# Performance work log

Measured on AMD Instinct MI355X. Metric: run time of the kernel, lower is better.

The kernel has to match this reference:

```python
import jax, jax.numpy as jnp
import numpy as np

B, S, DM, H, D = 2, 2048, 1024, 16, 64

def setup_inputs() -> dict:
    key = jax.random.key(0)
    ks = jax.random.split(key, 9)
    def g(k, shape, scale=0.02):
        return jax.random.normal(k, shape, dtype=jnp.float32) * scale
    return {
        "x":  jax.random.normal(ks[0], (B, S, DM), dtype=jnp.float32),
        "Wq": g(ks[1], (DM, H * D)), "bq": g(ks[2], (H * D,)),
        "Wk": g(ks[3], (DM, H * D)), "bk": g(ks[4], (H * D,)),
        "Wv": g(ks[5], (DM, H * D)), "bv": g(ks[6], (H * D,)),
        "Wo": g(ks[7], (H * D, DM)), "bo": g(ks[8], (DM,)),
    }

def reference(x, Wq, bq, Wk, bk, Wv, bv, Wo, bo):
    b, s, _ = x.shape
    # projections -> (B, H, S, D)
    q = (x @ Wq + bq).reshape(b, s, H, D).transpose(0, 2, 1, 3)
    k = (x @ Wk + bk).reshape(b, s, H, D).transpose(0, 2, 1, 3)
    v = (x @ Wv + bv).reshape(b, s, H, D).transpose(0, 2, 1, 3)
    # naive attention: full (B,H,S,S) scores, causal mask, softmax
    scores = jnp.einsum("bhqd,bhkd->bhqk", q, k) / jnp.sqrt(jnp.float32(D))
    causal = jnp.tril(jnp.ones((s, s), dtype=bool))
    scores = jnp.where(causal[None, None], scores, jnp.float32(-jnp.inf))
    weights = jax.nn.softmax(scores, axis=-1)
    out = jnp.einsum("bhqk,bhkd->bhqd", weights, v)  # (B,H,S,D)
    out = out.transpose(0, 2, 1, 3).reshape(b, s, H * D)
    return out @ Wo + bo  # dropout_p = 0 -> identity
```

## Files before the change

### kernel.cpp

```cpp
#include <hip/hip_runtime.h>
#include <hip/hip_bf16.h>

typedef __hip_bfloat16 bf16;
typedef __attribute__((ext_vector_type(8))) short bf16x8;
typedef __attribute__((ext_vector_type(4))) float f32x4;
typedef __attribute__((ext_vector_type(4))) unsigned int u32x4;

#define MFMA_BF16(a, b, c) __builtin_amdgcn_mfma_f32_16x16x32_bf16((a), (b), (c), 0, 0, 0)

static constexpr int B_  = 2;
static constexpr int S_  = 2048;
static constexpr int DM_ = 1024;
static constexpr int H_  = 16;
static constexpr int D_  = 64;
static constexpr int M_  = B_ * S_;

__device__ __forceinline__ void load16(const void* g, void* l) {
  __builtin_amdgcn_global_load_lds(
      (const __attribute__((address_space(1))) void*)g,
      (__attribute__((address_space(3))) void*)l, 16, 0, 0);
}

__device__ __forceinline__ unsigned int pack_bf16(float lo, float hi) {
  const unsigned int ul = __builtin_bit_cast(unsigned short, __float2bfloat16(lo));
  const unsigned int uh = __builtin_bit_cast(unsigned short, __float2bfloat16(hi));
  return (uh << 16) | ul;
}


__global__ void cvt_f32_bf16_kernel(const float* __restrict__ in,
                                    bf16* __restrict__ out, int n4) {
  int i = blockIdx.x * blockDim.x + threadIdx.x;
  if (i >= n4) return;
  float4 v = ((const float4*)in)[i];
  ushort4 u;
  u.x = __builtin_bit_cast(unsigned short, __float2bfloat16(v.x));
  u.y = __builtin_bit_cast(unsigned short, __float2bfloat16(v.y));
  u.z = __builtin_bit_cast(unsigned short, __float2bfloat16(v.z));
  u.w = __builtin_bit_cast(unsigned short, __float2bfloat16(v.w));
  ((ushort4*)out)[i] = u;
}

__global__ void transpose_cvt_kernel(const float* __restrict__ w0,
                                     const float* __restrict__ w1,
                                     const float* __restrict__ w2,
                                     const float* __restrict__ w3,
                                     bf16* __restrict__ o0, bf16* __restrict__ o1,
                                     bf16* __restrict__ o2, bf16* __restrict__ o3) {
  __shared__ float t[32][33];
  const float* in = blockIdx.z == 0 ? w0 : blockIdx.z == 1 ? w1 : blockIdx.z == 2 ? w2 : w3;
  bf16* out = blockIdx.z == 0 ? o0 : blockIdx.z == 1 ? o1 : blockIdx.z == 2 ? o2 : o3;
  int tx = threadIdx.x & 31;
  int ty = threadIdx.x >> 5;
  int r0 = blockIdx.y * 32;
  int c0 = blockIdx.x * 32;
#pragma unroll
  for (int yy = 0; yy < 32; yy += 8)
    t[ty + yy][tx] = in[(size_t)(r0 + ty + yy) * DM_ + c0 + tx];
  __syncthreads();
#pragma unroll
  for (int yy = 0; yy < 32; yy += 8)
    out[(size_t)(c0 + ty + yy) * DM_ + r0 + tx] = __float2bfloat16(t[tx][ty + yy]);
}

template <int MODE>
__global__ __launch_bounds__(256) void gemm_bt_kernel(
    const bf16* __restrict__ A, const bf16* __restrict__ Bt,
    const float* __restrict__ bias, const float* __restrict__ bias2,
    const float* __restrict__ bias3, void* __restrict__ out, int K) {
  __shared__ bf16 As[2][128 * 32];
  __shared__ bf16 Bs[2][128 * 32];
  const int tid = threadIdx.x;
  const int wid = tid >> 6, lane = tid & 63;
  const int g = lane >> 4, c = lane & 15;
  const int wr = wid >> 1, wc = wid & 1;
  const int bm = blockIdx.x, bn = blockIdx.y;

  f32x4 acc[4][4] = {};

  const char* Ag = (const char*)(A + (size_t)bm * 128 * K);
  const char* Bg = (const char*)(Bt + (size_t)bn * 128 * K);
  const int f0 = tid * 16, f1 = f0 + 4096;
  const int r0 = f0 >> 6, cb0 = f0 & 63;
  const int r1 = f1 >> 6;
  const size_t rowbytes = (size_t)K * 2;

  auto stage = [&](int kt, int bufi) {
    const size_t koff = (size_t)kt * 64;
    load16(Ag + (size_t)r0 * rowbytes + koff + cb0, (char*)As[bufi] + f0);
    load16(Ag + (size_t)r1 * rowbytes + koff + cb0, (char*)As[bufi] + f1);
    load16(Bg + (size_t)r0 * rowbytes + koff + cb0, (char*)Bs[bufi] + f0);
    load16(Bg + (size_t)r1 * rowbytes + koff + cb0, (char*)Bs[bufi] + f1);
  };

  const int NT = K / 32;
  stage(0, 0);
  int cur = 0;
#pragma unroll 1
  for (int kt = 0; kt < NT; ++kt) {
    if (kt + 1 < NT) {
      stage(kt + 1, cur ^ 1);
      asm volatile("s_waitcnt vmcnt(4)" ::: "memory");
    } else {
      asm volatile("s_waitcnt vmcnt(0)" ::: "memory");
    }
    __builtin_amdgcn_s_barrier();

    bf16x8 af[4], bfr[4];
#pragma unroll
    for (int mi = 0; mi < 4; ++mi)
      af[mi] = *(const bf16x8*)&As[cur][(wr * 64 + mi * 16 + c) * 32 + g * 8];
#pragma unroll
    for (int ni = 0; ni < 4; ++ni)
      bfr[ni] = *(const bf16x8*)&Bs[cur][(wc * 64 + ni * 16 + c) * 32 + g * 8];
    __builtin_amdgcn_s_setprio(1);
#pragma unroll
    for (int mi = 0; mi < 4; ++mi)
#pragma unroll
      for (int ni = 0; ni < 4; ++ni)
        acc[mi][ni] = MFMA_BF16(af[mi], bfr[ni], acc[mi][ni]);
    __builtin_amdgcn_s_setprio(0);

    if (kt + 1 < NT) __builtin_amdgcn_s_barrier();
    cur ^= 1;
  }

#pragma unroll
  for (int ni = 0; ni < 4; ++ni) {
    const int n_g = bn * 128 + wc * 64 + ni * 16 + c;
    float bv;
    if constexpr (MODE == 3) {
      const int proj = n_g >> 10, ncol = n_g & 1023;
      bv = proj == 0 ? bias[ncol] : proj == 1 ? bias2[ncol] : bias3[ncol];
    } else {
      bv = bias[n_g];
    }
#pragma unroll
    for (int mi = 0; mi < 4; ++mi) {
#pragma unroll
      for (int r = 0; r < 4; ++r) {
        const int m_g = bm * 128 + wr * 64 + mi * 16 + g * 4 + r;
        const float val = acc[mi][ni][r] + bv;
        if constexpr (MODE == 2) {
          ((float*)out)[(size_t)m_g * DM_ + n_g] = val;
        } else {
          const int proj = n_g >> 10, ncol = n_g & 1023;
          const int b = m_g >> 11, s = m_g & (S_ - 1);
          const int h = ncol >> 6, d = ncol & (D_ - 1);
          size_t idx = (size_t)proj * 4194304;
          if (proj < 2)
            idx += (((size_t)(b * H_ + h)) * S_ + s) * D_ + d;
          else
            idx += (((size_t)(b * H_ + h)) * D_ + d) * S_ + s;
          ((bf16*)out)[idx] = __float2bfloat16(val);
        }
      }
    }
  }
}

__global__ __launch_bounds__(256, 4) void flash_attn_kernel(
    const bf16* __restrict__ Q, const bf16* __restrict__ Kg,
    const bf16* __restrict__ Vt, bf16* __restrict__ Aout) {
  __shared__ bf16 Ks[2][64 * 64];
  __shared__ bf16 Vs[2][64 * 64];
  const int tid = threadIdx.x;
  const int w = tid >> 6, lane = tid & 63;
  const int g = lane >> 4, c = lane & 15;

  const int bid = blockIdx.x;
  const int xcd = bid & 7, loc = bid >> 3;
  const int bh = xcd * 4 + (loc & 3);
  const int j = 31 - (loc >> 2);
  const int t = j * 4 + w;
  const int b = bh >> 4, h = bh & (H_ - 1);

  const float ALPHA2 = 0.125f * 1.44269504f;
  const float THR2 = 11.5f;
  const float NEG_INF = -__builtin_inff();

  const char* Kbase = (const char*)(Kg + (size_t)bh * S_ * D_);
  const char* Vbase = (const char*)(Vt + (size_t)bh * D_ * S_);
  const int s0 = tid, s1 = tid + 256;
  const int sr0 = s0 >> 3, sq0 = ((s0 & 7) ^ (sr0 & 7)) << 4;
  const int sr1 = s1 >> 3, sq1 = ((s1 & 7) ^ (sr1 & 7)) << 4;

  const bf16* Qp = Q + ((size_t)bh * S_ + t * 16 + c) * D_;
  bf16x8 qf[2];
  qf[0] = *(const bf16x8*)&Qp[g * 8];
  qf[1] = *(const bf16x8*)&Qp[32 + g * 8];

  f32x4 o[4] = {};
  float m = -1000.0f;
  float lsum = 0.0f;

  const int rowlim = w * 16 + c;
  const int src0 = ((g & 1) * 2) * 16 + c;
  const int src1 = src0 + 16;
  const bool ghi = (g >= 2);
  const int cs = c & 7;
  int roff[2][4];
#pragma unroll
  for (int kk = 0; kk < 2; ++kk)
#pragma unroll
    for (int n = 0; n < 4; ++n)
      roff[kk][n] = n * 2048 + c * 128 + (((kk * 4 + g) ^ cs) << 4);

  {
    load16(Kbase + sr0 * 128 + sq0, (char*)Ks[0] + s0 * 16);
    load16(Kbase + sr1 * 128 + sq1, (char*)Ks[0] + s1 * 16);
    load16(Vbase + sr0 * 4096 + sq0, (char*)Vs[0] + s0 * 16);
    load16(Vbase + sr1 * 4096 + sq1, (char*)Vs[0] + s1 * 16);
  }
  __syncthreads();

  int cur = 0;
#pragma unroll 1
  for (int kv = 0; kv <= j; ++kv) {
    if (kv < j) {
      const char* Krow = Kbase + (size_t)(kv + 1) * 8192;
      const char* Vcol = Vbase + (size_t)(kv + 1) * 128;
      const int nb = cur ^ 1;
      load16(Krow + sr0 * 128 + sq0, (char*)Ks[nb] + s0 * 16);
      load16(Krow + sr1 * 128 + sq1, (char*)Ks[nb] + s1 * 16);
      load16(Vcol + sr0 * 4096 + sq0, (char*)Vs[nb] + s0 * 16);
      load16(Vcol + sr1 * 4096 + sq1, (char*)Vs[nb] + s1 * 16);
    }

    const char* Kt = (const char*)Ks[cur];
    const char* Vtile = (const char*)Vs[cur];
    bf16x8 kf[2][4];
#pragma unroll
    for (int kk = 0; kk < 2; ++kk)
#pragma unroll
      for (int n = 0; n < 4; ++n)
        kf[kk][n] = *(const bf16x8*)(Kt + roff[kk][n]);

    f32x4 st[4] = {};
    __builtin_amdgcn_s_setprio(1);
#pragma unroll
    for (int n = 0; n < 4; ++n) {
      st[n] = MFMA_BF16(kf[0][n], qf[0], st[n]);
      st[n] = MFMA_BF16(kf[1][n], qf[1], st[n]);
    }
    __builtin_amdgcn_s_setprio(0);

    bf16x8 vf[2][4];
#pragma unroll
    for (int kk = 0; kk < 2; ++kk)
#pragma unroll
      for (int n = 0; n < 4; ++n)
        vf[kk][n] = *(const bf16x8*)(Vtile + roff[kk][n]);

    float a[4][4];
#pragma unroll
    for (int n = 0; n < 4; ++n)
#pragma unroll
      for (int r = 0; r < 4; ++r)
        a[n][r] = fmaf(st[n][r], ALPHA2, -m);
    if (kv == j) {
#pragma unroll
      for (int n = 0; n < 4; ++n)
#pragma unroll
        for (int r = 0; r < 4; ++r)
          if (n * 16 + g * 4 + r > rowlim) a[n][r] = NEG_INF;
    }

    float dm;
    {
      float t0 = fmaxf(fmaxf(a[0][0], a[0][1]), fmaxf(a[0][2], a[0][3]));
      float t1 = fmaxf(fmaxf(a[1][0], a[1][1]), fmaxf(a[1][2], a[1][3]));
      float t2 = fmaxf(fmaxf(a[2][0], a[2][1]), fmaxf(a[2][2], a[2][3]));
      float t3 = fmaxf(fmaxf(a[3][0], a[3][1]), fmaxf(a[3][2], a[3][3]));
      dm = fmaxf(fmaxf(t0, t1), fmaxf(t2, t3));
    }
    dm = fmaxf(dm, __shfl_xor(dm, 16, 64));
    dm = fmaxf(dm, __shfl_xor(dm, 32, 64));

    if (__any(dm > THR2)) {
      const float sh = fmaxf(dm, 0.0f);
      const float sc = __builtin_amdgcn_exp2f(-sh);
      m += sh;
      lsum *= sc;
#pragma unroll
      for (int n = 0; n < 4; ++n)
#pragma unroll
        for (int r = 0; r < 4; ++r) o[n][r] *= sc;
#pragma unroll
      for (int n = 0; n < 4; ++n)
#pragma unroll
        for (int r = 0; r < 4; ++r) a[n][r] -= sh;
    }

    float p[4][4];
#pragma unroll
    for (int n = 0; n < 4; ++n)
#pragma unroll
      for (int r = 0; r < 4; ++r) p[n][r] = __builtin_amdgcn_exp2f(a[n][r]);
    {
      float q0 = (p[0][0] + p[0][1]) + (p[0][2] + p[0][3]);
      float q1 = (p[1][0] + p[1][1]) + (p[1][2] + p[1][3]);
      float q2 = (p[2][0] + p[2][1]) + (p[2][2] + p[2][3]);
      float q3 = (p[3][0] + p[3][1]) + (p[3][2] + p[3][3]);
      lsum += (q0 + q1) + (q2 + q3);
    }

    unsigned int dw[4][2];
#pragma unroll
    for (int n = 0; n < 4; ++n) {
      dw[n][0] = pack_bf16(p[n][0], p[n][1]);
      dw[n][1] = pack_bf16(p[n][2], p[n][3]);
    }

#pragma unroll
    for (int kk = 0; kk < 2; ++kk) {
      unsigned int bb[4];
      {
        unsigned int lo = __shfl(dw[kk * 2][0], src0, 64);
        unsigned int hi = __shfl(dw[kk * 2 + 1][0], src0, 64);
        bb[0] = ghi ? hi : lo;
      }
      {
        unsigned int lo = __shfl(dw[kk * 2][1], src0, 64);
        unsigned int hi = __shfl(dw[kk * 2 + 1][1], src0, 64);
        bb[1] = ghi ? hi : lo;
      }
      {
        unsigned int lo = __shfl(dw[kk * 2][0], src1, 64);
        unsigned int hi = __shfl(dw[kk * 2 + 1][0], src1, 64);
        bb[2] = ghi ? hi : lo;
      }
      {
        unsigned int lo = __shfl(dw[kk * 2][1], src1, 64);
        unsigned int hi = __shfl(dw[kk * 2 + 1][1], src1, 64);
        bb[3] = ghi ? hi : lo;
      }
      u32x4 bbv = {bb[0], bb[1], bb[2], bb[3]};
      bf16x8 pb = __builtin_bit_cast(bf16x8, bbv);
      __builtin_amdgcn_s_setprio(1);
#pragma unroll
      for (int n = 0; n < 4; ++n) o[n] = MFMA_BF16(vf[kk][n], pb, o[n]);
      __builtin_amdgcn_s_setprio(0);
    }

    __syncthreads();
    cur ^= 1;
  }

  lsum += __shfl_xor(lsum, 16, 64);
  lsum += __shfl_xor(lsum, 32, 64);
  const float inv = 1.0f / lsum;

  bf16* Arow = Aout + ((size_t)b * S_ + t * 16 + c) * (H_ * D_) + h * D_;
#pragma unroll
  for (int n = 0; n < 4; ++n) {
    ushort4 u;
    u.x = __builtin_bit_cast(unsigned short, __float2bfloat16(o[n][0] * inv));
    u.y = __builtin_bit_cast(unsigned short, __float2bfloat16(o[n][1] * inv));
    u.z = __builtin_bit_cast(unsigned short, __float2bfloat16(o[n][2] * inv));
    u.w = __builtin_bit_cast(unsigned short, __float2bfloat16(o[n][3] * inv));
    *(ushort4*)&Arow[n * 16 + g * 4] = u;
  }
}


extern "C" void kernel_launch(void* const* d_in, const int* in_sizes, int n_in,
                              void* d_out, int out_size, void* d_ws, size_t ws_size,
                              hipStream_t stream) {
  (void)in_sizes; (void)n_in; (void)out_size; (void)ws_size;
  const float* x  = (const float*)d_in[0];
  const float* Wq = (const float*)d_in[1];
  const float* bq = (const float*)d_in[2];
  const float* Wk = (const float*)d_in[3];
  const float* bk = (const float*)d_in[4];
  const float* Wv = (const float*)d_in[5];
  const float* bv = (const float*)d_in[6];
  const float* Wo = (const float*)d_in[7];
  const float* bo = (const float*)d_in[8];
  float* out = (float*)d_out;

  char* ws = (char*)d_ws;
  bf16* xb  = (bf16*)(ws);
  bf16* Wqt = (bf16*)(ws + (8u << 20));
  bf16* Wkt = (bf16*)(ws + (10u << 20));
  bf16* Wvt = (bf16*)(ws + (12u << 20));
  bf16* Wot = (bf16*)(ws + (14u << 20));
  bf16* Qb  = (bf16*)(ws + (16u << 20));
  bf16* Kb  = (bf16*)(ws + (24u << 20));
  bf16* Vtb = (bf16*)(ws + (32u << 20));
  bf16* Ab  = xb;

  cvt_f32_bf16_kernel<<<4096, 256, 0, stream>>>(x, xb, (M_ * DM_) / 4);
  transpose_cvt_kernel<<<dim3(32, 32, 4), 256, 0, stream>>>(
      Wq, Wk, Wv, Wo, Wqt, Wkt, Wvt, Wot);

  gemm_bt_kernel<3><<<dim3(32, 24), 256, 0, stream>>>(
      xb, Wqt, bq, bk, bv, (void*)Qb, DM_);

  flash_attn_kernel<<<dim3(1024), 256, 0, stream>>>(Qb, Kb, Vtb, Ab);

  gemm_bt_kernel<2><<<dim3(32, 8), 256, 0, stream>>>(
      Ab, Wot, bo, nullptr, nullptr, (void*)out, DM_);
}
```

Before: 121.6 us.

## Split flash attention blocks into 2-wave halves and drop KV double buffering

The attention kernel now launches 2048 blocks of 128 threads, each covering half of a 64-row query tile, in place of 1024 blocks of 256 threads. LDS use per block is halved by removing the double-buffered K/V tiles: each iteration loads the tile synchronously and then waits on a barrier. The aim is finer-grained scheduling and better load balance across the causal triangle, plus higher occupancy. The cost is that each K/V tile is loaded twice as often overall, and load latency is no longer hidden behind compute by prefetching.

```diff
diff --git a/kernel.cpp b/kernel.cpp
--- a/kernel.cpp
+++ b/kernel.cpp
@@ -159,11 +159,11 @@
   }
 }
 
-__global__ __launch_bounds__(256, 4) void flash_attn_kernel(
+__global__ __launch_bounds__(128, 5) void flash_attn_kernel(
     const bf16* __restrict__ Q, const bf16* __restrict__ Kg,
     const bf16* __restrict__ Vt, bf16* __restrict__ Aout) {
-  __shared__ bf16 Ks[2][64 * 64];
-  __shared__ bf16 Vs[2][64 * 64];
+  __shared__ bf16 Ks[64 * 64];
+  __shared__ bf16 Vs[64 * 64];
   const int tid = threadIdx.x;
   const int w = tid >> 6, lane = tid & 63;
   const int g = lane >> 4, c = lane & 15;
@@ -171,8 +171,10 @@
   const int bid = blockIdx.x;
   const int xcd = bid & 7, loc = bid >> 3;
   const int bh = xcd * 4 + (loc & 3);
-  const int j = 31 - (loc >> 2);
-  const int t = j * 4 + w;
+  const int hq = 63 - (loc >> 2);
+  const int j = hq >> 1;
+  const int half = hq & 1;
+  const int t = j * 4 + half * 2 + w;
   const int b = bh >> 4, h = bh & (H_ - 1);
 
   const float ALPHA2 = 0.125f * 1.44269504f;
@@ -181,9 +183,13 @@
 
   const char* Kbase = (const char*)(Kg + (size_t)bh * S_ * D_);
   const char* Vbase = (const char*)(Vt + (size_t)bh * D_ * S_);
-  const int s0 = tid, s1 = tid + 256;
-  const int sr0 = s0 >> 3, sq0 = ((s0 & 7) ^ (sr0 & 7)) << 4;
-  const int sr1 = s1 >> 3, sq1 = ((s1 & 7) ^ (sr1 & 7)) << 4;
+  int srk[4], sqk[4];
+#pragma unroll
+  for (int k = 0; k < 4; ++k) {
+    const int s = tid + k * 128;
+    srk[k] = s >> 3;
+    sqk[k] = ((s & 7) ^ (srk[k] & 7)) << 4;
+  }
 
   const bf16* Qp = Q + ((size_t)bh * S_ + t * 16 + c) * D_;
   bf16x8 qf[2];
@@ -194,7 +200,7 @@
   float m = -1000.0f;
   float lsum = 0.0f;
 
-  const int rowlim = w * 16 + c;
+  const int rowlim = (half * 2 + w) * 16 + c;
   const int src0 = ((g & 1) * 2) * 16 + c;
   const int src1 = src0 + 16;
   const bool ghi = (g >= 2);
@@ -206,35 +212,25 @@
     for (int n = 0; n < 4; ++n)
       roff[kk][n] = n * 2048 + c * 128 + (((kk * 4 + g) ^ cs) << 4);
 
-  {
-    load16(Kbase + sr0 * 128 + sq0, (char*)Ks[0] + s0 * 16);
-    load16(Kbase + sr1 * 128 + sq1, (char*)Ks[0] + s1 * 16);
-    load16(Vbase + sr0 * 4096 + sq0, (char*)Vs[0] + s0 * 16);
-    load16(Vbase + sr1 * 4096 + sq1, (char*)Vs[0] + s1 * 16);
-  }
-  __syncthreads();
-
-  int cur = 0;
 #pragma unroll 1
   for (int kv = 0; kv <= j; ++kv) {
-    if (kv < j) {
-      const char* Krow = Kbase + (size_t)(kv + 1) * 8192;
-      const char* Vcol = Vbase + (size_t)(kv + 1) * 128;
-      const int nb = cur ^ 1;
-      load16(Krow + sr0 * 128 + sq0, (char*)Ks[nb] + s0 * 16);
-      load16(Krow + sr1 * 128 + sq1, (char*)Ks[nb] + s1 * 16);
-      load16(Vcol + sr0 * 4096 + sq0, (char*)Vs[nb] + s0 * 16);
-      load16(Vcol + sr1 * 4096 + sq1, (char*)Vs[nb] + s1 * 16);
-    }
-
-    const char* Kt = (const char*)Ks[cur];
-    const char* Vtile = (const char*)Vs[cur];
+    {
+      const char* Krow = Kbase + (size_t)kv * 8192;
+      const char* Vcol = Vbase + (size_t)kv * 128;
+#pragma unroll
+      for (int k = 0; k < 4; ++k) {
+        load16(Krow + srk[k] * 128 + sqk[k], (char*)Ks + (tid + k * 128) * 16);
+        load16(Vcol + srk[k] * 4096 + sqk[k], (char*)Vs + (tid + k * 128) * 16);
+      }
+    }
+    __syncthreads();
+
     bf16x8 kf[2][4];
 #pragma unroll
     for (int kk = 0; kk < 2; ++kk)
 #pragma unroll
       for (int n = 0; n < 4; ++n)
-        kf[kk][n] = *(const bf16x8*)(Kt + roff[kk][n]);
+        kf[kk][n] = *(const bf16x8*)((const char*)Ks + roff[kk][n]);
 
     f32x4 st[4] = {};
     __builtin_amdgcn_s_setprio(1);
@@ -250,28 +246,28 @@
     for (int kk = 0; kk < 2; ++kk)
 #pragma unroll
       for (int n = 0; n < 4; ++n)
-        vf[kk][n] = *(const bf16x8*)(Vtile + roff[kk][n]);
-
-    float a[4][4];
+        vf[kk][n] = *(const bf16x8*)((const char*)Vs + roff[kk][n]);
+
+    float aa[4][4];
 #pragma unroll
     for (int n = 0; n < 4; ++n)
 #pragma unroll
       for (int r = 0; r < 4; ++r)
-        a[n][r] = fmaf(st[n][r], ALPHA2, -m);
+        aa[n][r] = fmaf(st[n][r], ALPHA2, -m);
     if (kv == j) {
 #pragma unroll
       for (int n = 0; n < 4; ++n)
 #pragma unroll
         for (int r = 0; r < 4; ++r)
-          if (n * 16 + g * 4 + r > rowlim) a[n][r] = NEG_INF;
+          if (n * 16 + g * 4 + r > rowlim) aa[n][r] = NEG_INF;
     }
 
     float dm;
     {
-      float t0 = fmaxf(fmaxf(a[0][0], a[0][1]), fmaxf(a[0][2], a[0][3]));
-      float t1 = fmaxf(fmaxf(a[1][0], a[1][1]), fmaxf(a[1][2], a[1][3]));
-      float t2 = fmaxf(fmaxf(a[2][0], a[2][1]), fmaxf(a[2][2], a[2][3]));
-      float t3 = fmaxf(fmaxf(a[3][0], a[3][1]), fmaxf(a[3][2], a[3][3]));
+      float t0 = fmaxf(fmaxf(aa[0][0], aa[0][1]), fmaxf(aa[0][2], aa[0][3]));
+      float t1 = fmaxf(fmaxf(aa[1][0], aa[1][1]), fmaxf(aa[1][2], aa[1][3]));
+      float t2 = fmaxf(fmaxf(aa[2][0], aa[2][1]), fmaxf(aa[2][2], aa[2][3]));
+      float t3 = fmaxf(fmaxf(aa[3][0], aa[3][1]), fmaxf(aa[3][2], aa[3][3]));
       dm = fmaxf(fmaxf(t0, t1), fmaxf(t2, t3));
     }
     dm = fmaxf(dm, __shfl_xor(dm, 16, 64));
@@ -289,14 +285,14 @@
 #pragma unroll
       for (int n = 0; n < 4; ++n)
 #pragma unroll
-        for (int r = 0; r < 4; ++r) a[n][r] -= sh;
+        for (int r = 0; r < 4; ++r) aa[n][r] -= sh;
     }
 
     float p[4][4];
 #pragma unroll
     for (int n = 0; n < 4; ++n)
 #pragma unroll
-      for (int r = 0; r < 4; ++r) p[n][r] = __builtin_amdgcn_exp2f(a[n][r]);
+      for (int r = 0; r < 4; ++r) p[n][r] = __builtin_amdgcn_exp2f(aa[n][r]);
     {
       float q0 = (p[0][0] + p[0][1]) + (p[0][2] + p[0][3]);
       float q1 = (p[1][0] + p[1][1]) + (p[1][2] + p[1][3]);
@@ -344,7 +340,6 @@
     }
 
     __syncthreads();
-    cur ^= 1;
   }
 
   lsum += __shfl_xor(lsum, 16, 64);
@@ -397,7 +392,7 @@
   gemm_bt_kernel<3><<<dim3(32, 24), 256, 0, stream>>>(
       xb, Wqt, bq, bk, bv, (void*)Qb, DM_);
 
-  flash_attn_kernel<<<dim3(1024), 256, 0, stream>>>(Qb, Kb, Vtb, Ab);
+  flash_attn_kernel<<<dim3(2048), 128, 0, stream>>>(Qb, Kb, Vtb, Ab);
 
   gemm_bt_kernel<2><<<dim3(32, 8), 256, 0, stream>>>(
       Ab, Wot, bo, nullptr, nullptr, (void*)out, DM_);
```

Result: slower. 137.3 us (+12.9%).

## Add 256x256-tile QKV GEMM kernel with swizzled LDS and XCD-aware block remap

Applied to the files above, without the earlier changes.

Replaces the 128x128 QKV projection GEMM with a dedicated 512-thread kernel using 256x256 output tiles, 64-wide K steps, XOR-swizzled LDS layout and loads of the next stage interleaved across four sub-phases. Blocks are remapped so consecutive tiles land on the same XCD for better L2 reuse. The larger tile cuts global reloads of A and B and the swizzle avoids LDS bank conflicts. In exchange it uses 128 KB of LDS per block and many accumulator registers, which limits occupancy and gives only 192 blocks. The output GEMM template is simplified and a flash-attention variable is renamed.

```diff
diff --git a/kernel.cpp b/kernel.cpp
--- a/kernel.cpp
+++ b/kernel.cpp
@@ -63,11 +63,119 @@
     out[(size_t)(c0 + ty + yy) * DM_ + r0 + tx] = __float2bfloat16(t[tx][ty + yy]);
 }
 
-template <int MODE>
+__global__ __launch_bounds__(512, 2) void gemm256_qkv_kernel(
+    const bf16* __restrict__ A, const bf16* __restrict__ Bt,
+    const float* __restrict__ bias, const float* __restrict__ bias2,
+    const float* __restrict__ bias3, bf16* __restrict__ out) {
+  __shared__ bf16 As[2][256 * 64];
+  __shared__ bf16 Bs[2][256 * 64];
+  const int tid = threadIdx.x;
+  const int wid = tid >> 6, lane = tid & 63;
+  const int g = lane >> 4, c = lane & 15;
+  const int wr = wid >> 2, wc = wid & 3;
+
+  const int orig = blockIdx.x;
+  const int wgid = (orig & 7) * 24 + (orig >> 3);
+  const int bm = wgid & 15, bn = wgid >> 4;
+
+  const char* Ag = (const char*)(A + (size_t)bm * 256 * 1024);
+  const char* Bg = (const char*)(Bt + (size_t)bn * 256 * 1024);
+
+  f32x4 acc[8][4] = {};
+
+  auto stage2 = [&](int kt, int bufi, int pp) {
+#pragma unroll
+    for (int l = 0; l < 2; ++l) {
+      const int k = pp * 2 + l;
+      const int s = tid + (k & 3) * 512;
+      const int sr = s >> 3;
+      const int sq = ((s & 7) ^ (sr & 7)) << 4;
+      if (k < 4)
+        load16(Ag + (size_t)sr * 2048 + kt * 128 + sq, (char*)As[bufi] + s * 16);
+      else
+        load16(Bg + (size_t)sr * 2048 + kt * 128 + sq, (char*)Bs[bufi] + s * 16);
+    }
+  };
+
+#pragma unroll
+  for (int pp = 0; pp < 4; ++pp) stage2(0, 0, pp);
+
+  const int c7 = c & 7;
+  int cur = 0;
+#pragma unroll 1
+  for (int kt = 0; kt < 16; ++kt) {
+    if (kt < 15) {
+      stage2(kt + 1, cur ^ 1, 0);
+      asm volatile("s_waitcnt vmcnt(2)" ::: "memory");
+    } else {
+      asm volatile("s_waitcnt vmcnt(0)" ::: "memory");
+    }
+    __builtin_amdgcn_s_barrier();
+
+#pragma unroll
+    for (int p = 0; p < 4; ++p) {
+      const int qr = p >> 1, qc = p & 1;
+      bf16x8 af[4][2], bfr[2][2];
+#pragma unroll
+      for (int mi = 0; mi < 4; ++mi) {
+        const int rb = (wr * 128 + qr * 64 + mi * 16 + c) * 128;
+#pragma unroll
+        for (int kk = 0; kk < 2; ++kk)
+          af[mi][kk] = *(const bf16x8*)((const char*)As[cur] + rb +
+                                        (((kk * 4 + g) ^ c7) << 4));
+      }
+#pragma unroll
+      for (int ni = 0; ni < 2; ++ni) {
+        const int rb = (wc * 64 + qc * 32 + ni * 16 + c) * 128;
+#pragma unroll
+        for (int kk = 0; kk < 2; ++kk)
+          bfr[ni][kk] = *(const bf16x8*)((const char*)Bs[cur] + rb +
+                                         (((kk * 4 + g) ^ c7) << 4));
+      }
+      if (p < 3 && kt < 15) stage2(kt + 1, cur ^ 1, p + 1);
+      __builtin_amdgcn_s_barrier();
+      __builtin_amdgcn_s_setprio(1);
+#pragma unroll
+      for (int mi = 0; mi < 4; ++mi)
+#pragma unroll
+        for (int ni = 0; ni < 2; ++ni)
+#pragma unroll
+          for (int kk = 0; kk < 2; ++kk)
+            acc[qr * 4 + mi][qc * 2 + ni] =
+                MFMA_BF16(af[mi][kk], bfr[ni][kk], acc[qr * 4 + mi][qc * 2 + ni]);
+      __builtin_amdgcn_s_setprio(0);
+      __builtin_amdgcn_s_barrier();
+    }
+    cur ^= 1;
+  }
+
+#pragma unroll
+  for (int ni = 0; ni < 4; ++ni) {
+    const int n_g = bn * 256 + wc * 64 + ni * 16 + c;
+    const int proj = n_g >> 10, ncol = n_g & 1023;
+    const float bv = proj == 0 ? bias[ncol] : proj == 1 ? bias2[ncol] : bias3[ncol];
+    const int h = ncol >> 6, d = ncol & (D_ - 1);
+#pragma unroll
+    for (int mi = 0; mi < 8; ++mi) {
+#pragma unroll
+      for (int rr = 0; rr < 4; ++rr) {
+        const int m_g = bm * 256 + wr * 128 + mi * 16 + g * 4 + rr;
+        const float val = acc[mi][ni][rr] + bv;
+        const int b = m_g >> 11, s = m_g & (S_ - 1);
+        size_t idx = (size_t)proj * 4194304;
+        if (proj < 2)
+          idx += (((size_t)(b * H_ + h)) * S_ + s) * D_ + d;
+        else
+          idx += (((size_t)(b * H_ + h)) * D_ + d) * S_ + s;
+        out[idx] = __float2bfloat16(val);
+      }
+    }
+  }
+}
+
 __global__ __launch_bounds__(256) void gemm_bt_kernel(
     const bf16* __restrict__ A, const bf16* __restrict__ Bt,
-    const float* __restrict__ bias, const float* __restrict__ bias2,
-    const float* __restrict__ bias3, void* __restrict__ out, int K) {
+    const float* __restrict__ bias, float* __restrict__ out, int K) {
   __shared__ bf16 As[2][128 * 32];
   __shared__ bf16 Bs[2][128 * 32];
   const int tid = threadIdx.x;
@@ -128,32 +236,13 @@
 #pragma unroll
   for (int ni = 0; ni < 4; ++ni) {
     const int n_g = bn * 128 + wc * 64 + ni * 16 + c;
-    float bv;
-    if constexpr (MODE == 3) {
-      const int proj = n_g >> 10, ncol = n_g & 1023;
-      bv = proj == 0 ? bias[ncol] : proj == 1 ? bias2[ncol] : bias3[ncol];
-    } else {
-      bv = bias[n_g];
-    }
+    const float bv = bias[n_g];
 #pragma unroll
     for (int mi = 0; mi < 4; ++mi) {
 #pragma unroll
       for (int r = 0; r < 4; ++r) {
         const int m_g = bm * 128 + wr * 64 + mi * 16 + g * 4 + r;
-        const float val = acc[mi][ni][r] + bv;
-        if constexpr (MODE == 2) {
-          ((float*)out)[(size_t)m_g * DM_ + n_g] = val;
-        } else {
-          const int proj = n_g >> 10, ncol = n_g & 1023;
-          const int b = m_g >> 11, s = m_g & (S_ - 1);
-          const int h = ncol >> 6, d = ncol & (D_ - 1);
-          size_t idx = (size_t)proj * 4194304;
-          if (proj < 2)
-            idx += (((size_t)(b * H_ + h)) * S_ + s) * D_ + d;
-          else
-            idx += (((size_t)(b * H_ + h)) * D_ + d) * S_ + s;
-          ((bf16*)out)[idx] = __float2bfloat16(val);
-        }
+        out[(size_t)m_g * DM_ + n_g] = acc[mi][ni][r] + bv;
       }
     }
   }
@@ -252,26 +341,26 @@
       for (int n = 0; n < 4; ++n)
         vf[kk][n] = *(const bf16x8*)(Vtile + roff[kk][n]);
 
-    float a[4][4];
+    float aa[4][4];
 #pragma unroll
     for (int n = 0; n < 4; ++n)
 #pragma unroll
       for (int r = 0; r < 4; ++r)
-        a[n][r] = fmaf(st[n][r], ALPHA2, -m);
+        aa[n][r] = fmaf(st[n][r], ALPHA2, -m);
     if (kv == j) {
 #pragma unroll
       for (int n = 0; n < 4; ++n)
 #pragma unroll
         for (int r = 0; r < 4; ++r)
-          if (n * 16 + g * 4 + r > rowlim) a[n][r] = NEG_INF;
+          if (n * 16 + g * 4 + r > rowlim) aa[n][r] = NEG_INF;
     }
 
     float dm;
     {
-      float t0 = fmaxf(fmaxf(a[0][0], a[0][1]), fmaxf(a[0][2], a[0][3]));
-      float t1 = fmaxf(fmaxf(a[1][0], a[1][1]), fmaxf(a[1][2], a[1][3]));
-      float t2 = fmaxf(fmaxf(a[2][0], a[2][1]), fmaxf(a[2][2], a[2][3]));
-      float t3 = fmaxf(fmaxf(a[3][0], a[3][1]), fmaxf(a[3][2], a[3][3]));
+      float t0 = fmaxf(fmaxf(aa[0][0], aa[0][1]), fmaxf(aa[0][2], aa[0][3]));
+      float t1 = fmaxf(fmaxf(aa[1][0], aa[1][1]), fmaxf(aa[1][2], aa[1][3]));
+      float t2 = fmaxf(fmaxf(aa[2][0], aa[2][1]), fmaxf(aa[2][2], aa[2][3]));
+      float t3 = fmaxf(fmaxf(aa[3][0], aa[3][1]), fmaxf(aa[3][2], aa[3][3]));
       dm = fmaxf(fmaxf(t0, t1), fmaxf(t2, t3));
     }
     dm = fmaxf(dm, __shfl_xor(dm, 16, 64));
@@ -289,14 +378,14 @@
 #pragma unroll
       for (int n = 0; n < 4; ++n)
 #pragma unroll
-        for (int r = 0; r < 4; ++r) a[n][r] -= sh;
+        for (int r = 0; r < 4; ++r) aa[n][r] -= sh;
     }
 
     float p[4][4];
 #pragma unroll
     for (int n = 0; n < 4; ++n)
 #pragma unroll
-      for (int r = 0; r < 4; ++r) p[n][r] = __builtin_amdgcn_exp2f(a[n][r]);
+      for (int r = 0; r < 4; ++r) p[n][r] = __builtin_amdgcn_exp2f(aa[n][r]);
     {
       float q0 = (p[0][0] + p[0][1]) + (p[0][2] + p[0][3]);
       float q1 = (p[1][0] + p[1][1]) + (p[1][2] + p[1][3]);
@@ -394,11 +483,10 @@
   transpose_cvt_kernel<<<dim3(32, 32, 4), 256, 0, stream>>>(
       Wq, Wk, Wv, Wo, Wqt, Wkt, Wvt, Wot);
 
-  gemm_bt_kernel<3><<<dim3(32, 24), 256, 0, stream>>>(
-      xb, Wqt, bq, bk, bv, (void*)Qb, DM_);
+  gemm256_qkv_kernel<<<dim3(192), 512, 0, stream>>>(
+      xb, Wqt, bq, bk, bv, Qb);
 
   flash_attn_kernel<<<dim3(1024), 256, 0, stream>>>(Qb, Kb, Vtb, Ab);
 
-  gemm_bt_kernel<2><<<dim3(32, 8), 256, 0, stream>>>(
-      Ab, Wot, bo, nullptr, nullptr, (void*)out, DM_);
-}
+  gemm_bt_kernel<<<dim3(32, 8), 256, 0, stream>>>(Ab, Wot, bo, out, DM_);
+}
```

Result: slower. 149.8 us (+23.2%).
